# Performance work log

Measured on AMD Instinct MI355X. Metric: run time of the kernel, lower is better.

The kernel has to match this reference:

```python
import jax, jax.numpy as jnp
import numpy as np

N_I, N_O = 100000, 50000   # indivi / org node counts
F = 32                     # node feature dim (both types)
EA = 8                     # edge feature dim
E = 100000                 # edges per relation


def setup_inputs() -> dict:
    key = jax.random.key(0)
    ks = jax.random.split(key, 20)
    s = 0.05
    return {
        "x_indivi": jax.random.normal(ks[0], (N_I, F), jnp.float32),
        "x_org": jax.random.normal(ks[1], (N_O, F), jnp.float32),
        "edge_src_oi": jax.random.randint(ks[2], (E,), 0, N_O),
        "edge_dst_oi": jax.random.randint(ks[3], (E,), 0, N_I),
        "edge_attr_oi": jax.random.normal(ks[4], (E, EA), jnp.float32),
        "edge_src_io": jax.random.randint(ks[5], (E,), 0, N_I),
        "edge_dst_io": jax.random.randint(ks[6], (E,), 0, N_O),
        "edge_attr_io": jax.random.normal(ks[7], (E, EA), jnp.float32),
        "Wm_oi": jax.random.normal(ks[8], (EA, F * F), jnp.float32) * s,
        "bm_oi": jax.random.normal(ks[9], (F * F,), jnp.float32) * s,
        "Wr_oi": jax.random.normal(ks[10], (F, F), jnp.float32) * s,
        "b_oi": jax.random.normal(ks[11], (F,), jnp.float32) * s,
        "Wm_io": jax.random.normal(ks[12], (EA, F * F), jnp.float32) * s,
        "bm_io": jax.random.normal(ks[13], (F * F,), jnp.float32) * s,
        "Wr_io": jax.random.normal(ks[14], (F, F), jnp.float32) * s,
        "b_io": jax.random.normal(ks[15], (F,), jnp.float32) * s,
        "Wm2": jax.random.normal(ks[16], (EA, F * 1), jnp.float32) * s,
        "bm2": jax.random.normal(ks[17], (F * 1,), jnp.float32) * s,
        "Wr2": jax.random.normal(ks[18], (F, 1), jnp.float32) * s,
        "b2": jax.random.normal(ks[19], (1,), jnp.float32) * s,
    }


def nnconv(x_src, x_dst, src, dst, eattr, Wm, bm, Wr, b, f_out):
    # per-edge weight matrix from edge attributes: [E, F_src, f_out]
    w = (eattr @ Wm + bm).reshape(-1, x_src.shape[1], f_out)
    msg = jnp.einsum('ei,eio->eo', x_src[src], w)          # gather + per-edge matmul
    agg = jax.ops.segment_sum(msg, dst, num_segments=x_dst.shape[0])  # scatter-add
    return agg + x_dst @ Wr + b                             # root weight + bias


def reference(x_indivi, x_org, edge_src_oi, edge_dst_oi, edge_attr_oi,
              edge_src_io, edge_dst_io, edge_attr_io,
              Wm_oi, bm_oi, Wr_oi, b_oi,
              Wm_io, bm_io, Wr_io, b_io,
              Wm2, bm2, Wr2, b2):
    # Inner layer: hetero NNConv, aggr='sum' across relations per dst type
    h_indivi = jax.nn.sigmoid(
        nnconv(x_org, x_indivi, edge_src_oi, edge_dst_oi, edge_attr_oi,
               Wm_oi, bm_oi, Wr_oi, b_oi, F))
    h_org = jax.nn.sigmoid(
        nnconv(x_indivi, x_org, edge_src_io, edge_dst_io, edge_attr_io,
               Wm_io, bm_io, Wr_io, b_io, F))
    # Output layer: only relations with dst == 'indivi', out_channels = 1
    out = nnconv(h_org, h_indivi, edge_src_oi, edge_dst_oi, edge_attr_oi,
                 Wm2, bm2, Wr2, b2, 1)
    return jax.nn.sigmoid(out)
```

## Files before the change

kernel.cpp:

```cpp
#include <hip/hip_runtime.h>
#include <math.h>

#define NI 100000
#define NO 50000
#define NE 100000
#define NB (NI + NO)
#define TOTE (2 * NE)

#define OFF_WRT_OI    0
#define OFF_WRT_IO    1024
#define OFF_WFRAG     2048
#define OFF_Y2Z2      11264
#define OFF_SCANNED   611264
#define OFF_BLOCKSUM  761280
#define OFF_BLOCKPREF 761920
#define OFF_SORTED    762560
#define OFF_DSTS      962560
#define OFF_ACC       1162560
#define OFF_CNT       5962560
#define OFF_CNT2      6112576

static constexpr int B_EDGE = (NE + 255) / 256;
static constexpr int B_IND  = (NI + 255) / 256;
static constexpr int B_ORG  = (NO + 255) / 256;
static constexpr int SCAN_BLOCKS = (NB + 255) / 256;

static constexpr int FB_HIST_END  = 782;
static constexpr int FB_ZERO_END  = 1038;
static constexpr int FB_WRT_END   = 1046;
static constexpr int FB_WFRAG_END = 1055;

typedef __attribute__((ext_vector_type(8))) short short8;
typedef __attribute__((ext_vector_type(4))) float f32x4;

__device__ __forceinline__ float sigmoidf_fast(float x) {
    return 1.0f / (1.0f + __expf(-x));
}
__device__ __forceinline__ unsigned f2bf(float f) {
    unsigned u = __float_as_uint(f);
    return (u + 0x7FFFu + ((u >> 16) & 1u)) >> 16;
}
__device__ __forceinline__ unsigned pack_trunc(float lo, float hi) {
    return __builtin_amdgcn_perm(__float_as_uint(hi), __float_as_uint(lo), 0x07060302u);
}

__global__ __launch_bounds__(256) void k_front(
    const int* __restrict__ dst_oi, const int* __restrict__ dst_io,
    const float* __restrict__ Wm_oi, const float* __restrict__ bm_oi, const float* __restrict__ Wr_oi,
    const float* __restrict__ Wm_io, const float* __restrict__ bm_io, const float* __restrict__ Wr_io,
    float* __restrict__ ws, int* __restrict__ cnt)
{
    int b = blockIdx.x;
    if (b < FB_HIST_END) {
        bool is_io = b >= B_EDGE;
        int e = (is_io ? (b - B_EDGE) : b) * 256 + threadIdx.x;
        if (e >= NE) return;
        int cd = is_io ? (NI + dst_io[e]) : dst_oi[e];
        atomicAdd(&cnt[cd], 1);
    } else if (b < FB_ZERO_END) {
        int idx = (b - FB_HIST_END) * 256 + threadIdx.x;
        float4* a4 = (float4*)(ws + OFF_ACC);
        for (int q = idx; q < 1200000; q += 65536)
            a4[q] = make_float4(0.f, 0.f, 0.f, 0.f);
    } else if (b < FB_WRT_END) {
        int u = (b - FB_ZERO_END) * 256 + threadIdx.x;
        if (u < 1024)      ws[OFF_WRT_OI + u] = Wr_oi[(u & 31) * 32 + (u >> 5)];
        else if (u < 2048) { int v = u - 1024; ws[OFF_WRT_IO + v] = Wr_io[(v & 31) * 32 + (v >> 5)]; }
    } else {
        int u = (b - FB_WRT_END) * 256 + threadIdx.x;
        if (u >= 2304) return;
        int rel = u >= 1152;
        int v = u - rel * 1152;
        int lane = v & 63;
        int fi = v >> 6;
        int a = fi >> 1;
        int nt = fi & 1;
        int quad = lane >> 4;
        int n = nt * 16 + (lane & 15);
        const float* Wm = rel ? Wm_io : Wm_oi;
        const float* bm = rel ? bm_io : bm_oi;
        unsigned pk[4];
        #pragma unroll
        for (int d = 0; d < 4; d++) {
            int k0 = quad * 8 + 2 * d;
            float vlo = (a < 8) ? Wm[a * 1024 + k0 * 32 + n]       : bm[k0 * 32 + n];
            float vhi = (a < 8) ? Wm[a * 1024 + (k0 + 1) * 32 + n] : bm[(k0 + 1) * 32 + n];
            pk[d] = f2bf(vlo) | (f2bf(vhi) << 16);
        }
        uint4* wf = (uint4*)(ws + OFF_WFRAG);
        wf[((rel * 9 + a) * 2 + nt) * 64 + lane] = make_uint4(pk[0], pk[1], pk[2], pk[3]);
    }
}

__global__ __launch_bounds__(256) void k_scan_block(
    const int* __restrict__ cnt, int* __restrict__ scanned, int* __restrict__ blocksum)
{
    int d = blockIdx.x * 256 + threadIdx.x;
    int v = (d < NB) ? cnt[d] : 0;
    int lane = threadIdx.x & 63, wv = threadIdx.x >> 6;
    int s = v;
    #pragma unroll
    for (int off = 1; off < 64; off <<= 1) {
        int t = __shfl_up(s, off);
        if (lane >= off) s += t;
    }
    __shared__ int wsum[4];
    if (lane == 63) wsum[wv] = s;
    __syncthreads();
    int add = 0;
    for (int w = 0; w < wv; w++) add += wsum[w];
    int incl = s + add;
    scanned[d] = incl - v;
    if (threadIdx.x == 255) blocksum[blockIdx.x] = incl;
}

__global__ __launch_bounds__(1024) void k_scan_top(
    const int* __restrict__ blocksum, int* __restrict__ blockpref)
{
    __shared__ int L[1024];
    int t = threadIdx.x;
    int v = (t < SCAN_BLOCKS) ? blocksum[t] : 0;
    L[t] = v;
    __syncthreads();
    for (int off = 1; off < 1024; off <<= 1) {
        int u = (t >= off) ? L[t - off] : 0;
        __syncthreads();
        L[t] += u;
        __syncthreads();
    }
    if (t < SCAN_BLOCKS) blockpref[t] = L[t] - v;
}

__global__ __launch_bounds__(256) void k_scatter(
    const int* __restrict__ dst_oi, const int* __restrict__ dst_io,
    const int* __restrict__ scanned, const int* __restrict__ blockpref,
    int* __restrict__ cnt2, int* __restrict__ sorted_eid, int* __restrict__ dstsorted)
{
    bool is_io = blockIdx.x >= B_EDGE;
    int e = (is_io ? (blockIdx.x - B_EDGE) : blockIdx.x) * 256 + threadIdx.x;
    if (e >= NE) return;
    int cd = is_io ? (NI + dst_io[e]) : dst_oi[e];
    int base = scanned[cd] + blockpref[cd >> 8];
    int pos = base + atomicAdd(&cnt2[cd], 1);
    sorted_eid[pos] = e;
    dstsorted[pos] = cd;
}

__global__ __launch_bounds__(256) void k_edge(
    const int* __restrict__ src_oi, const float* __restrict__ attr_oi,
    const int* __restrict__ src_io, const float* __restrict__ attr_io,
    const float* __restrict__ x_ind, const float* __restrict__ x_org,
    const float* __restrict__ ws,
    const int* __restrict__ sorted_eid, const int* __restrict__ dstsorted,
    float* __restrict__ acc)
{
    __shared__ uint4 xstage[4][256];
    __shared__ float stage[256 * 36];

    bool is_io = blockIdx.x >= B_EDGE;
    int blockStart = is_io ? (NE + (blockIdx.x - B_EDGE) * 256) : (blockIdx.x * 256);
    int relEnd = is_io ? TOTE : NE;
    int tid = threadIdx.x;
    int wave = tid >> 6, lane = tid & 63, quad = lane >> 4;
    int p = blockStart + tid;
    bool act = p < relEnd;

    const int*   srcA  = is_io ? src_io : src_oi;
    const float* attrA = is_io ? attr_io : attr_oi;
    const float* xsrc  = is_io ? x_ind : x_org;

    const uint4* wfr = ((const uint4*)(ws + OFF_WFRAG)) + (is_io ? 1152 : 0);
    uint4 bf[9][2];
    #pragma unroll
    for (int a = 0; a < 9; a++) {
        #pragma unroll
        for (int nt = 0; nt < 2; nt++)
            bf[a][nt] = wfr[((a * 2 + nt) * 64) + lane];
    }

    int cd = -1;
    float ar[9];
    ar[8] = 1.0f;
    if (act) {
        cd = dstsorted[p];
        int e = sorted_eid[p];
        int s = srcA[e];
        {
            const float4* ap = (const float4*)(attrA + e * 8);
            float4 v0 = ap[0], v1 = ap[1];
            ar[0] = v0.x; ar[1] = v0.y; ar[2] = v0.z; ar[3] = v0.w;
            ar[4] = v1.x; ar[5] = v1.y; ar[6] = v1.z; ar[7] = v1.w;
        }
        const float4* xp = (const float4*)(xsrc + s * 32);
        #pragma unroll
        for (int q = 0; q < 4; q++) {
            float4 v0 = xp[2 * q], v1 = xp[2 * q + 1];
            uint4 pk;
            pk.x = pack_trunc(v0.x, v0.y);
            pk.y = pack_trunc(v0.z, v0.w);
            pk.z = pack_trunc(v1.x, v1.y);
            pk.w = pack_trunc(v1.z, v1.w);
            xstage[wave][q * 64 + lane] = pk;
        }
    }

    f32x4 zero4 = {0.f, 0.f, 0.f, 0.f};
    #pragma unroll
    for (int mtile = 0; mtile < 4; mtile++) {
        uint4 araw = xstage[wave][quad * 64 + mtile * 16 + (lane & 15)];
        short8 af = *(short8*)&araw;
        float mm0[4] = {0.f, 0.f, 0.f, 0.f};
        float mm1[4] = {0.f, 0.f, 0.f, 0.f};
        #pragma unroll
        for (int a = 0; a < 9; a++) {
            f32x4 t0 = __builtin_amdgcn_mfma_f32_16x16x32_bf16(af, *(short8*)&bf[a][0], zero4, 0, 0, 0);
            f32x4 t1 = __builtin_amdgcn_mfma_f32_16x16x32_bf16(af, *(short8*)&bf[a][1], zero4, 0, 0, 0);
            #pragma unroll
            for (int r = 0; r < 4; r++) {
                int m = mtile * 16 + quad * 4 + r;
                float av = __shfl(ar[a], m, 64);
                mm0[r] = fmaf(av, t0[r], mm0[r]);
                mm1[r] = fmaf(av, t1[r], mm1[r]);
            }
        }
        #pragma unroll
        for (int r = 0; r < 4; r++) {
            int row = wave * 64 + mtile * 16 + quad * 4 + r;
            stage[row * 36 + (lane & 15)]      = mm0[r];
            stage[row * 36 + 16 + (lane & 15)] = mm1[r];
        }
    }
    __syncthreads();

    bool head = act && (p == blockStart || dstsorted[p - 1] != cd);
    if (head) {
        float msg[32];
        const float4* rrow0 = (const float4*)(stage + tid * 36);
        #pragma unroll
        for (int j = 0; j < 8; j++) {
            float4 v = rrow0[j];
            msg[j * 4 + 0] = v.x; msg[j * 4 + 1] = v.y;
            msg[j * 4 + 2] = v.z; msg[j * 4 + 3] = v.w;
        }
        int blockEnd = min(blockStart + 256, relEnd);
        int q = p + 1;
        while (q < blockEnd && dstsorted[q] == cd) {
            const float4* rrow = (const float4*)(stage + (q - blockStart) * 36);
            #pragma unroll
            for (int j = 0; j < 8; j++) {
                float4 v = rrow[j];
                msg[j * 4 + 0] += v.x; msg[j * 4 + 1] += v.y;
                msg[j * 4 + 2] += v.z; msg[j * 4 + 3] += v.w;
            }
            q++;
        }
        bool openR = (q == blockEnd) && (q < TOTE) && (dstsorted[q] == cd);
        bool openL = (p == blockStart) && (p > 0) && (dstsorted[p - 1] == cd);
        float* dp = acc + (size_t)cd * 32;
        if (openL || openR) {
            #pragma unroll
            for (int o = 0; o < 32; o++) atomicAdd(dp + o, msg[o]);
        } else {
            float4* dp4 = (float4*)dp;
            #pragma unroll
            for (int j = 0; j < 8; j++)
                dp4[j] = make_float4(msg[j * 4 + 0], msg[j * 4 + 1], msg[j * 4 + 2], msg[j * 4 + 3]);
        }
    }
}

__global__ __launch_bounds__(256) void k_finish(
    const float* __restrict__ x_ind, const float* __restrict__ x_org,
    const float* __restrict__ ws, const float* __restrict__ acc,
    const float* __restrict__ b_oi, const float* __restrict__ b_io,
    const float* __restrict__ Wm2, const float* __restrict__ bm2,
    const float* __restrict__ Wr2, const float* __restrict__ b2,
    float* __restrict__ y2z2, float* __restrict__ out)
{
    bool is_org = blockIdx.x >= B_IND;
    int n = (is_org ? (blockIdx.x - B_IND) : blockIdx.x) * 256 + threadIdx.x;
    int N = is_org ? NO : NI;
    if (n >= N) return;
    int cd = is_org ? (NI + n) : n;

    const float* x    = is_org ? x_org : x_ind;
    const float* WrT  = ws + (is_org ? OFF_WRT_IO : OFF_WRT_OI);
    const float* bias = is_org ? b_io : b_oi;

    float xr[32];
    const float4* xp = (const float4*)(x + n * 32);
    #pragma unroll
    for (int q = 0; q < 8; q++) {
        float4 v = xp[q];
        xr[q * 4 + 0] = v.x; xr[q * 4 + 1] = v.y; xr[q * 4 + 2] = v.z; xr[q * 4 + 3] = v.w;
    }
    float h[32];
    const float4* aprow = (const float4*)(acc + (size_t)cd * 32);
    #pragma unroll
    for (int q = 0; q < 8; q++) {
        float4 v = aprow[q];
        h[q * 4 + 0] = v.x; h[q * 4 + 1] = v.y; h[q * 4 + 2] = v.z; h[q * 4 + 3] = v.w;
    }
    #pragma unroll 4
    for (int o = 0; o < 32; o++) {
        float s = bias[o] + h[o];
        #pragma unroll
        for (int i = 0; i < 32; i++) s = fmaf(xr[i], WrT[o * 32 + i], s);
        h[o] = sigmoidf_fast(s);
    }
    if (!is_org) {
        float s = b2[0];
        #pragma unroll
        for (int i = 0; i < 32; i++) s = fmaf(h[i], Wr2[i], s);
        out[n] = s;
    } else {
        float z2 = 0.0f;
        #pragma unroll
        for (int i = 0; i < 32; i++) z2 = fmaf(h[i], bm2[i], z2);
        float* yz = y2z2 + n * 12;
        yz[0] = z2;
        #pragma unroll
        for (int a = 0; a < 8; a++) {
            float s = 0.0f;
            #pragma unroll
            for (int i = 0; i < 32; i++) s = fmaf(h[i], Wm2[a * 32 + i], s);
            yz[1 + a] = s;
        }
    }
}

__global__ __launch_bounds__(256) void k_out(
    const int* __restrict__ src_oi, const float* __restrict__ attr_oi,
    const int* __restrict__ scanned, const int* __restrict__ blockpref,
    const int* __restrict__ sorted_eid, const float* __restrict__ y2z2,
    float* __restrict__ out)
{
    int d = blockIdx.x * 256 + threadIdx.x;
    if (d >= NI) return;
    int base = scanned[d] + blockpref[d >> 8];
    int next = scanned[d + 1] + blockpref[(d + 1) >> 8];
    float t = out[d];
    for (int p = base; p < next; p++) {
        int e = sorted_eid[p];
        int s = src_oi[e];
        const float* yz = y2z2 + s * 12;
        const float4* ap = (const float4*)(attr_oi + e * 8);
        float4 a0 = ap[0], a1 = ap[1];
        float m = yz[0];
        m = fmaf(a0.x, yz[1], m); m = fmaf(a0.y, yz[2], m);
        m = fmaf(a0.z, yz[3], m); m = fmaf(a0.w, yz[4], m);
        m = fmaf(a1.x, yz[5], m); m = fmaf(a1.y, yz[6], m);
        m = fmaf(a1.z, yz[7], m); m = fmaf(a1.w, yz[8], m);
        t += m;
    }
    out[d] = sigmoidf_fast(t);
}

extern "C" void kernel_launch(void* const* d_in, const int* in_sizes, int n_in,
                              void* d_out, int out_size, void* d_ws, size_t ws_size,
                              hipStream_t stream)
{
    const float* x_ind   = (const float*)d_in[0];
    const float* x_org   = (const float*)d_in[1];
    const int*   src_oi  = (const int*)d_in[2];
    const int*   dst_oi  = (const int*)d_in[3];
    const float* attr_oi = (const float*)d_in[4];
    const int*   src_io  = (const int*)d_in[5];
    const int*   dst_io  = (const int*)d_in[6];
    const float* attr_io = (const float*)d_in[7];
    const float* Wm_oi   = (const float*)d_in[8];
    const float* bm_oi   = (const float*)d_in[9];
    const float* Wr_oi   = (const float*)d_in[10];
    const float* b_oi    = (const float*)d_in[11];
    const float* Wm_io   = (const float*)d_in[12];
    const float* bm_io   = (const float*)d_in[13];
    const float* Wr_io   = (const float*)d_in[14];
    const float* b_io    = (const float*)d_in[15];
    const float* Wm2     = (const float*)d_in[16];
    const float* bm2     = (const float*)d_in[17];
    const float* Wr2     = (const float*)d_in[18];
    const float* b2      = (const float*)d_in[19];

    float* ws        = (float*)d_ws;
    float* y2z2      = ws + OFF_Y2Z2;
    int*   scanned   = (int*)(ws + OFF_SCANNED);
    int*   blocksum  = (int*)(ws + OFF_BLOCKSUM);
    int*   blockpref = (int*)(ws + OFF_BLOCKPREF);
    int*   sorted    = (int*)(ws + OFF_SORTED);
    int*   dsts      = (int*)(ws + OFF_DSTS);
    float* acc       = ws + OFF_ACC;
    int*   cnt       = (int*)(ws + OFF_CNT);
    int*   cnt2      = (int*)(ws + OFF_CNT2);
    float* out       = (float*)d_out;

    hipMemsetAsync(ws + OFF_CNT, 0, (size_t)(2 * 150016) * 4, stream);

    k_front<<<FB_WFRAG_END, 256, 0, stream>>>(
        dst_oi, dst_io, Wm_oi, bm_oi, Wr_oi, Wm_io, bm_io, Wr_io, ws, cnt);

    k_scan_block<<<SCAN_BLOCKS, 256, 0, stream>>>(cnt, scanned, blocksum);

    k_scan_top<<<1, 1024, 0, stream>>>(blocksum, blockpref);

    k_scatter<<<2 * B_EDGE, 256, 0, stream>>>(
        dst_oi, dst_io, scanned, blockpref, cnt2, sorted, dsts);

    k_edge<<<2 * B_EDGE, 256, 0, stream>>>(
        src_oi, attr_oi, src_io, attr_io, x_ind, x_org, ws, sorted, dsts, acc);

    k_finish<<<B_IND + B_ORG, 256, 0, stream>>>(
        x_ind, x_org, ws, acc, b_oi, b_io, Wm2, bm2, Wr2, b2, y2z2, out);

    k_out<<<B_IND, 256, 0, stream>>>(
        src_oi, attr_oi, scanned, blockpref, sorted, y2z2, out);
}
```

Measured before the change: 184.2 us.

## Fuse scan passes, reuse histogram ranks, and fold indivi finish into output kernel

The histogram kernel now records each edge's atomic rank, so the scatter kernel no longer needs a second atomic counter pass or a second zeroed counter array. The two-level scan becomes a single kernel in which the last block, found through an atomic ticket, scans the block sums. The indivi half of the finish kernel moves into the output kernel, which drops the intermediate out write and read. This cuts launches, atomics and memset size, at the cost of a rank buffer and a heavier per-thread output kernel.

```diff
diff --git a/kernel.cpp b/kernel.cpp
--- a/kernel.cpp
+++ b/kernel.cpp
@@ -16,9 +16,10 @@
 #define OFF_BLOCKPREF 761920
 #define OFF_SORTED    762560
 #define OFF_DSTS      962560
-#define OFF_ACC       1162560
-#define OFF_CNT       5962560
-#define OFF_CNT2      6112576
+#define OFF_RANK      1162560
+#define OFF_ACC       1362560
+#define OFF_CNT       6162560
+#define OFF_TICKET    6312576
 
 static constexpr int B_EDGE = (NE + 255) / 256;
 static constexpr int B_IND  = (NI + 255) / 256;
@@ -48,7 +49,7 @@
     const int* __restrict__ dst_oi, const int* __restrict__ dst_io,
     const float* __restrict__ Wm_oi, const float* __restrict__ bm_oi, const float* __restrict__ Wr_oi,
     const float* __restrict__ Wm_io, const float* __restrict__ bm_io, const float* __restrict__ Wr_io,
-    float* __restrict__ ws, int* __restrict__ cnt)
+    float* __restrict__ ws, int* __restrict__ cnt, int* __restrict__ rank)
 {
     int b = blockIdx.x;
     if (b < FB_HIST_END) {
@@ -56,7 +57,7 @@
         int e = (is_io ? (b - B_EDGE) : b) * 256 + threadIdx.x;
         if (e >= NE) return;
         int cd = is_io ? (NI + dst_io[e]) : dst_oi[e];
-        atomicAdd(&cnt[cd], 1);
+        rank[is_io ? NE + e : e] = atomicAdd(&cnt[cd], 1);
     } else if (b < FB_ZERO_END) {
         int idx = (b - FB_HIST_END) * 256 + threadIdx.x;
         float4* a4 = (float4*)(ws + OFF_ACC);
@@ -92,8 +93,9 @@
     }
 }
 
-__global__ __launch_bounds__(256) void k_scan_block(
-    const int* __restrict__ cnt, int* __restrict__ scanned, int* __restrict__ blocksum)
+__global__ __launch_bounds__(256) void k_scan(
+    const int* __restrict__ cnt, int* __restrict__ scanned,
+    int* __restrict__ blocksum, int* __restrict__ blockpref, int* __restrict__ ticket)
 {
     int d = blockIdx.x * 256 + threadIdx.x;
     int v = (d < NB) ? cnt[d] : 0;
@@ -109,39 +111,55 @@
     __syncthreads();
     int add = 0;
     for (int w = 0; w < wv; w++) add += wsum[w];
-    int incl = s + add;
-    scanned[d] = incl - v;
-    if (threadIdx.x == 255) blocksum[blockIdx.x] = incl;
-}
-
-__global__ __launch_bounds__(1024) void k_scan_top(
-    const int* __restrict__ blocksum, int* __restrict__ blockpref)
-{
-    __shared__ int L[1024];
+    scanned[d] = s + add - v;
+
+    __shared__ int isLast;
+    if (threadIdx.x == 0) {
+        int total = wsum[0] + wsum[1] + wsum[2] + wsum[3];
+        blocksum[blockIdx.x] = total;
+        __threadfence();
+        isLast = (atomicAdd(ticket, 1) == (int)gridDim.x - 1);
+    }
+    __syncthreads();
+    if (!isLast) return;
+    __threadfence();
+
+    __shared__ int L[768];
     int t = threadIdx.x;
-    int v = (t < SCAN_BLOCKS) ? blocksum[t] : 0;
-    L[t] = v;
+    #pragma unroll
+    for (int j = 0; j < 3; j++) {
+        int i = t * 3 + j;
+        L[t * 3 + j] = (i < SCAN_BLOCKS) ? blocksum[i] : 0;
+    }
     __syncthreads();
-    for (int off = 1; off < 1024; off <<= 1) {
-        int u = (t >= off) ? L[t - off] : 0;
-        __syncthreads();
-        L[t] += u;
-        __syncthreads();
-    }
-    if (t < SCAN_BLOCKS) blockpref[t] = L[t] - v;
+    int s0 = L[t * 3], s1 = s0 + L[t * 3 + 1], s2 = s1 + L[t * 3 + 2];
+    int sc = s2;
+    #pragma unroll
+    for (int off = 1; off < 64; off <<= 1) {
+        int u = __shfl_up(sc, off);
+        if (lane >= off) sc += u;
+    }
+    __shared__ int wsum2[4];
+    if (lane == 63) wsum2[wv] = sc;
+    __syncthreads();
+    int add2 = 0;
+    for (int w = 0; w < wv; w++) add2 += wsum2[w];
+    int excl = sc + add2 - s2;
+    if (t * 3     < SCAN_BLOCKS) blockpref[t * 3]     = excl;
+    if (t * 3 + 1 < SCAN_BLOCKS) blockpref[t * 3 + 1] = excl + s0;
+    if (t * 3 + 2 < SCAN_BLOCKS) blockpref[t * 3 + 2] = excl + s1;
 }
 
 __global__ __launch_bounds__(256) void k_scatter(
     const int* __restrict__ dst_oi, const int* __restrict__ dst_io,
     const int* __restrict__ scanned, const int* __restrict__ blockpref,
-    int* __restrict__ cnt2, int* __restrict__ sorted_eid, int* __restrict__ dstsorted)
+    const int* __restrict__ rank, int* __restrict__ sorted_eid, int* __restrict__ dstsorted)
 {
     bool is_io = blockIdx.x >= B_EDGE;
     int e = (is_io ? (blockIdx.x - B_EDGE) : blockIdx.x) * 256 + threadIdx.x;
     if (e >= NE) return;
     int cd = is_io ? (NI + dst_io[e]) : dst_oi[e];
-    int base = scanned[cd] + blockpref[cd >> 8];
-    int pos = base + atomicAdd(&cnt2[cd], 1);
+    int pos = scanned[cd] + blockpref[cd >> 8] + rank[is_io ? NE + e : e];
     sorted_eid[pos] = e;
     dstsorted[pos] = cd;
 }
@@ -269,26 +287,19 @@
     }
 }
 
-__global__ __launch_bounds__(256) void k_finish(
-    const float* __restrict__ x_ind, const float* __restrict__ x_org,
-    const float* __restrict__ ws, const float* __restrict__ acc,
-    const float* __restrict__ b_oi, const float* __restrict__ b_io,
+__global__ __launch_bounds__(256) void k_finish_org(
+    const float* __restrict__ x_org, const float* __restrict__ ws, const float* __restrict__ acc,
+    const float* __restrict__ b_io,
     const float* __restrict__ Wm2, const float* __restrict__ bm2,
-    const float* __restrict__ Wr2, const float* __restrict__ b2,
-    float* __restrict__ y2z2, float* __restrict__ out)
-{
-    bool is_org = blockIdx.x >= B_IND;
-    int n = (is_org ? (blockIdx.x - B_IND) : blockIdx.x) * 256 + threadIdx.x;
-    int N = is_org ? NO : NI;
-    if (n >= N) return;
-    int cd = is_org ? (NI + n) : n;
-
-    const float* x    = is_org ? x_org : x_ind;
-    const float* WrT  = ws + (is_org ? OFF_WRT_IO : OFF_WRT_OI);
-    const float* bias = is_org ? b_io : b_oi;
+    float* __restrict__ y2z2)
+{
+    int n = blockIdx.x * 256 + threadIdx.x;
+    if (n >= NO) return;
+    int cd = NI + n;
+    const float* WrT = ws + OFF_WRT_IO;
 
     float xr[32];
-    const float4* xp = (const float4*)(x + n * 32);
+    const float4* xp = (const float4*)(x_org + n * 32);
     #pragma unroll
     for (int q = 0; q < 8; q++) {
         float4 v = xp[q];
@@ -303,33 +314,29 @@
     }
     #pragma unroll 4
     for (int o = 0; o < 32; o++) {
-        float s = bias[o] + h[o];
+        float s = b_io[o] + h[o];
         #pragma unroll
         for (int i = 0; i < 32; i++) s = fmaf(xr[i], WrT[o * 32 + i], s);
         h[o] = sigmoidf_fast(s);
     }
-    if (!is_org) {
-        float s = b2[0];
-        #pragma unroll
-        for (int i = 0; i < 32; i++) s = fmaf(h[i], Wr2[i], s);
-        out[n] = s;
-    } else {
-        float z2 = 0.0f;
-        #pragma unroll
-        for (int i = 0; i < 32; i++) z2 = fmaf(h[i], bm2[i], z2);
-        float* yz = y2z2 + n * 12;
-        yz[0] = z2;
-        #pragma unroll
-        for (int a = 0; a < 8; a++) {
-            float s = 0.0f;
-            #pragma unroll
-            for (int i = 0; i < 32; i++) s = fmaf(h[i], Wm2[a * 32 + i], s);
-            yz[1 + a] = s;
-        }
+    float z2 = 0.0f;
+    #pragma unroll
+    for (int i = 0; i < 32; i++) z2 = fmaf(h[i], bm2[i], z2);
+    float* yz = y2z2 + n * 12;
+    yz[0] = z2;
+    #pragma unroll
+    for (int a = 0; a < 8; a++) {
+        float s = 0.0f;
+        #pragma unroll
+        for (int i = 0; i < 32; i++) s = fmaf(h[i], Wm2[a * 32 + i], s);
+        yz[1 + a] = s;
     }
 }
 
 __global__ __launch_bounds__(256) void k_out(
+    const float* __restrict__ x_ind, const float* __restrict__ ws, const float* __restrict__ acc,
+    const float* __restrict__ b_oi,
+    const float* __restrict__ Wr2, const float* __restrict__ b2,
     const int* __restrict__ src_oi, const float* __restrict__ attr_oi,
     const int* __restrict__ scanned, const int* __restrict__ blockpref,
     const int* __restrict__ sorted_eid, const float* __restrict__ y2z2,
@@ -337,9 +344,33 @@
 {
     int d = blockIdx.x * 256 + threadIdx.x;
     if (d >= NI) return;
+    const float* WrT = ws + OFF_WRT_OI;
+
+    float xr[32];
+    const float4* xp = (const float4*)(x_ind + d * 32);
+    #pragma unroll
+    for (int q = 0; q < 8; q++) {
+        float4 v = xp[q];
+        xr[q * 4 + 0] = v.x; xr[q * 4 + 1] = v.y; xr[q * 4 + 2] = v.z; xr[q * 4 + 3] = v.w;
+    }
+    float h[32];
+    const float4* aprow = (const float4*)(acc + (size_t)d * 32);
+    #pragma unroll
+    for (int q = 0; q < 8; q++) {
+        float4 v = aprow[q];
+        h[q * 4 + 0] = v.x; h[q * 4 + 1] = v.y; h[q * 4 + 2] = v.z; h[q * 4 + 3] = v.w;
+    }
+    float t = b2[0];
+    #pragma unroll 4
+    for (int o = 0; o < 32; o++) {
+        float s = b_oi[o] + h[o];
+        #pragma unroll
+        for (int i = 0; i < 32; i++) s = fmaf(xr[i], WrT[o * 32 + i], s);
+        t = fmaf(sigmoidf_fast(s), Wr2[o], t);
+    }
+
     int base = scanned[d] + blockpref[d >> 8];
     int next = scanned[d + 1] + blockpref[(d + 1) >> 8];
-    float t = out[d];
     for (int p = base; p < next; p++) {
         int e = sorted_eid[p];
         int s = src_oi[e];
@@ -388,29 +419,29 @@
     int*   blockpref = (int*)(ws + OFF_BLOCKPREF);
     int*   sorted    = (int*)(ws + OFF_SORTED);
     int*   dsts      = (int*)(ws + OFF_DSTS);
+    int*   rank      = (int*)(ws + OFF_RANK);
     float* acc       = ws + OFF_ACC;
     int*   cnt       = (int*)(ws + OFF_CNT);
-    int*   cnt2      = (int*)(ws + OFF_CNT2);
+    int*   ticket    = (int*)(ws + OFF_TICKET);
     float* out       = (float*)d_out;
 
-    hipMemsetAsync(ws + OFF_CNT, 0, (size_t)(2 * 150016) * 4, stream);
+    hipMemsetAsync(ws + OFF_CNT, 0, (size_t)(150016 + 16) * 4, stream);
 
     k_front<<<FB_WFRAG_END, 256, 0, stream>>>(
-        dst_oi, dst_io, Wm_oi, bm_oi, Wr_oi, Wm_io, bm_io, Wr_io, ws, cnt);
-
-    k_scan_block<<<SCAN_BLOCKS, 256, 0, stream>>>(cnt, scanned, blocksum);
-
-    k_scan_top<<<1, 1024, 0, stream>>>(blocksum, blockpref);
+        dst_oi, dst_io, Wm_oi, bm_oi, Wr_oi, Wm_io, bm_io, Wr_io, ws, cnt, rank);
+
+    k_scan<<<SCAN_BLOCKS, 256, 0, stream>>>(cnt, scanned, blocksum, blockpref, ticket);
 
     k_scatter<<<2 * B_EDGE, 256, 0, stream>>>(
-        dst_oi, dst_io, scanned, blockpref, cnt2, sorted, dsts);
+        dst_oi, dst_io, scanned, blockpref, rank, sorted, dsts);
 
     k_edge<<<2 * B_EDGE, 256, 0, stream>>>(
         src_oi, attr_oi, src_io, attr_io, x_ind, x_org, ws, sorted, dsts, acc);
 
-    k_finish<<<B_IND + B_ORG, 256, 0, stream>>>(
-        x_ind, x_org, ws, acc, b_oi, b_io, Wm2, bm2, Wr2, b2, y2z2, out);
+    k_finish_org<<<B_ORG, 256, 0, stream>>>(
+        x_org, ws, acc, b_io, Wm2, bm2, y2z2);
 
     k_out<<<B_IND, 256, 0, stream>>>(
-        src_oi, attr_oi, scanned, blockpref, sorted, y2z2, out);
-}
+        x_ind, ws, acc, b_oi, Wr2, b2, src_oi, attr_oi,
+        scanned, blockpref, sorted, y2z2, out);
+}
```

Result: slower. 202.3 us (+9.8%).

## Replace counting-sort CSR with atomic linked lists and per-edge message buffer

Applied to the files above, without the earlier changes.

Drops the histogram, two-level scan and scatter kernels that built a destination-sorted edge order. Instead, the message kernel pushes each edge onto a per-destination linked list with atomicExch and writes its 32-float message to a global buffer. Per-node kernels then walk the lists to sum messages, and the root and bias math is fused into the org and output kernels. This cuts several launches and the sort passes, at the cost of writing and re-reading a 25.6MB message buffer, serial pointer-chasing gathers per node, and nondeterministic summation order.

```diff
diff --git a/kernel.cpp b/kernel.cpp
--- a/kernel.cpp
+++ b/kernel.cpp
@@ -7,28 +7,16 @@
 #define NB (NI + NO)
 #define TOTE (2 * NE)
 
-#define OFF_WRT_OI    0
-#define OFF_WRT_IO    1024
-#define OFF_WFRAG     2048
-#define OFF_Y2Z2      11264
-#define OFF_SCANNED   611264
-#define OFF_BLOCKSUM  761280
-#define OFF_BLOCKPREF 761920
-#define OFF_SORTED    762560
-#define OFF_DSTS      962560
-#define OFF_ACC       1162560
-#define OFF_CNT       5962560
-#define OFF_CNT2      6112576
+#define OFF_WFRAG   0
+#define OFF_Y2Z2    9216
+#define OFF_HEAD    609216
+#define OFF_NXT     759232
+#define OFF_MSG     959232
 
 static constexpr int B_EDGE = (NE + 255) / 256;
 static constexpr int B_IND  = (NI + 255) / 256;
 static constexpr int B_ORG  = (NO + 255) / 256;
-static constexpr int SCAN_BLOCKS = (NB + 255) / 256;
-
-static constexpr int FB_HIST_END  = 782;
-static constexpr int FB_ZERO_END  = 1038;
-static constexpr int FB_WRT_END   = 1046;
-static constexpr int FB_WFRAG_END = 1055;
+static constexpr int B_INIT = (NB + 2304 + 255) / 256;
 
 typedef __attribute__((ext_vector_type(8))) short short8;
 typedef __attribute__((ext_vector_type(4))) float f32x4;
@@ -44,30 +32,17 @@
     return __builtin_amdgcn_perm(__float_as_uint(hi), __float_as_uint(lo), 0x07060302u);
 }
 
-__global__ __launch_bounds__(256) void k_front(
-    const int* __restrict__ dst_oi, const int* __restrict__ dst_io,
-    const float* __restrict__ Wm_oi, const float* __restrict__ bm_oi, const float* __restrict__ Wr_oi,
-    const float* __restrict__ Wm_io, const float* __restrict__ bm_io, const float* __restrict__ Wr_io,
-    float* __restrict__ ws, int* __restrict__ cnt)
-{
-    int b = blockIdx.x;
-    if (b < FB_HIST_END) {
-        bool is_io = b >= B_EDGE;
-        int e = (is_io ? (b - B_EDGE) : b) * 256 + threadIdx.x;
-        if (e >= NE) return;
-        int cd = is_io ? (NI + dst_io[e]) : dst_oi[e];
-        atomicAdd(&cnt[cd], 1);
-    } else if (b < FB_ZERO_END) {
-        int idx = (b - FB_HIST_END) * 256 + threadIdx.x;
-        float4* a4 = (float4*)(ws + OFF_ACC);
-        for (int q = idx; q < 1200000; q += 65536)
-            a4[q] = make_float4(0.f, 0.f, 0.f, 0.f);
-    } else if (b < FB_WRT_END) {
-        int u = (b - FB_ZERO_END) * 256 + threadIdx.x;
-        if (u < 1024)      ws[OFF_WRT_OI + u] = Wr_oi[(u & 31) * 32 + (u >> 5)];
-        else if (u < 2048) { int v = u - 1024; ws[OFF_WRT_IO + v] = Wr_io[(v & 31) * 32 + (v >> 5)]; }
+__global__ __launch_bounds__(256) void k_init(
+    const float* __restrict__ Wm_oi, const float* __restrict__ bm_oi,
+    const float* __restrict__ Wm_io, const float* __restrict__ bm_io,
+    float* __restrict__ ws)
+{
+    int idx = blockIdx.x * 256 + threadIdx.x;
+    int* head = (int*)(ws + OFF_HEAD);
+    if (idx < NB) {
+        head[idx] = -1;
     } else {
-        int u = (b - FB_WRT_END) * 256 + threadIdx.x;
+        int u = idx - NB;
         if (u >= 2304) return;
         int rel = u >= 1152;
         int v = u - rel * 1152;
@@ -92,80 +67,30 @@
     }
 }
 
-__global__ __launch_bounds__(256) void k_scan_block(
-    const int* __restrict__ cnt, int* __restrict__ scanned, int* __restrict__ blocksum)
-{
-    int d = blockIdx.x * 256 + threadIdx.x;
-    int v = (d < NB) ? cnt[d] : 0;
-    int lane = threadIdx.x & 63, wv = threadIdx.x >> 6;
-    int s = v;
-    #pragma unroll
-    for (int off = 1; off < 64; off <<= 1) {
-        int t = __shfl_up(s, off);
-        if (lane >= off) s += t;
-    }
-    __shared__ int wsum[4];
-    if (lane == 63) wsum[wv] = s;
-    __syncthreads();
-    int add = 0;
-    for (int w = 0; w < wv; w++) add += wsum[w];
-    int incl = s + add;
-    scanned[d] = incl - v;
-    if (threadIdx.x == 255) blocksum[blockIdx.x] = incl;
-}
-
-__global__ __launch_bounds__(1024) void k_scan_top(
-    const int* __restrict__ blocksum, int* __restrict__ blockpref)
-{
-    __shared__ int L[1024];
-    int t = threadIdx.x;
-    int v = (t < SCAN_BLOCKS) ? blocksum[t] : 0;
-    L[t] = v;
-    __syncthreads();
-    for (int off = 1; off < 1024; off <<= 1) {
-        int u = (t >= off) ? L[t - off] : 0;
-        __syncthreads();
-        L[t] += u;
-        __syncthreads();
-    }
-    if (t < SCAN_BLOCKS) blockpref[t] = L[t] - v;
-}
-
-__global__ __launch_bounds__(256) void k_scatter(
-    const int* __restrict__ dst_oi, const int* __restrict__ dst_io,
-    const int* __restrict__ scanned, const int* __restrict__ blockpref,
-    int* __restrict__ cnt2, int* __restrict__ sorted_eid, int* __restrict__ dstsorted)
-{
-    bool is_io = blockIdx.x >= B_EDGE;
-    int e = (is_io ? (blockIdx.x - B_EDGE) : blockIdx.x) * 256 + threadIdx.x;
-    if (e >= NE) return;
-    int cd = is_io ? (NI + dst_io[e]) : dst_oi[e];
-    int base = scanned[cd] + blockpref[cd >> 8];
-    int pos = base + atomicAdd(&cnt2[cd], 1);
-    sorted_eid[pos] = e;
-    dstsorted[pos] = cd;
-}
-
-__global__ __launch_bounds__(256) void k_edge(
-    const int* __restrict__ src_oi, const float* __restrict__ attr_oi,
-    const int* __restrict__ src_io, const float* __restrict__ attr_io,
+__global__ __launch_bounds__(256) void k_msg(
+    const int* __restrict__ src_oi, const int* __restrict__ dst_oi, const float* __restrict__ attr_oi,
+    const int* __restrict__ src_io, const int* __restrict__ dst_io, const float* __restrict__ attr_io,
     const float* __restrict__ x_ind, const float* __restrict__ x_org,
-    const float* __restrict__ ws,
-    const int* __restrict__ sorted_eid, const int* __restrict__ dstsorted,
-    float* __restrict__ acc)
+    float* __restrict__ ws)
 {
     __shared__ uint4 xstage[4][256];
     __shared__ float stage[256 * 36];
 
+    int* head  = (int*)(ws + OFF_HEAD);
+    int* nxt   = (int*)(ws + OFF_NXT);
+    float* msg = ws + OFF_MSG;
+
     bool is_io = blockIdx.x >= B_EDGE;
-    int blockStart = is_io ? (NE + (blockIdx.x - B_EDGE) * 256) : (blockIdx.x * 256);
+    int blockStart = is_io ? (NE + ((int)blockIdx.x - B_EDGE) * 256) : ((int)blockIdx.x * 256);
     int relEnd = is_io ? TOTE : NE;
     int tid = threadIdx.x;
     int wave = tid >> 6, lane = tid & 63, quad = lane >> 4;
     int p = blockStart + tid;
     bool act = p < relEnd;
+    int e = p - (is_io ? NE : 0);
 
     const int*   srcA  = is_io ? src_io : src_oi;
+    const int*   dstA  = is_io ? dst_io : dst_oi;
     const float* attrA = is_io ? attr_io : attr_oi;
     const float* xsrc  = is_io ? x_ind : x_org;
 
@@ -178,12 +103,9 @@
             bf[a][nt] = wfr[((a * 2 + nt) * 64) + lane];
     }
 
-    int cd = -1;
     float ar[9];
     ar[8] = 1.0f;
     if (act) {
-        cd = dstsorted[p];
-        int e = sorted_eid[p];
         int s = srcA[e];
         {
             const float4* ap = (const float4*)(attrA + e * 8);
@@ -202,6 +124,9 @@
             pk.w = pack_trunc(v1.z, v1.w);
             xstage[wave][q * 64 + lane] = pk;
         }
+        int cd = is_io ? (NI + dstA[e]) : dstA[e];
+        int old = atomicExch(&head[cd], p);
+        nxt[p] = old;
     }
 
     f32x4 zero4 = {0.f, 0.f, 0.f, 0.f};
@@ -232,116 +157,93 @@
     }
     __syncthreads();
 
-    bool head = act && (p == blockStart || dstsorted[p - 1] != cd);
-    if (head) {
-        float msg[32];
-        const float4* rrow0 = (const float4*)(stage + tid * 36);
+    if (act) {
+        const float4* srow = (const float4*)(stage + tid * 36);
+        float4* mrow = (float4*)(msg + (size_t)p * 32);
+        #pragma unroll
+        for (int j = 0; j < 8; j++) mrow[j] = srow[j];
+    }
+}
+
+__global__ __launch_bounds__(256) void k_org(
+    const float* __restrict__ x_org, const float* __restrict__ ws,
+    const float* __restrict__ Wr_io, const float* __restrict__ b_io,
+    const float* __restrict__ Wm2, const float* __restrict__ bm2,
+    float* __restrict__ y2z2)
+{
+    int n = blockIdx.x * 256 + threadIdx.x;
+    if (n >= NO) return;
+    const int* head  = (const int*)(ws + OFF_HEAD);
+    const int* nxt   = (const int*)(ws + OFF_NXT);
+    const float* msg = ws + OFF_MSG;
+
+    float ms[32];
+    #pragma unroll
+    for (int o = 0; o < 32; o++) ms[o] = 0.0f;
+    for (int e = head[NI + n]; e != -1; e = nxt[e]) {
+        const float4* mr = (const float4*)(msg + (size_t)e * 32);
         #pragma unroll
         for (int j = 0; j < 8; j++) {
-            float4 v = rrow0[j];
-            msg[j * 4 + 0] = v.x; msg[j * 4 + 1] = v.y;
-            msg[j * 4 + 2] = v.z; msg[j * 4 + 3] = v.w;
-        }
-        int blockEnd = min(blockStart + 256, relEnd);
-        int q = p + 1;
-        while (q < blockEnd && dstsorted[q] == cd) {
-            const float4* rrow = (const float4*)(stage + (q - blockStart) * 36);
-            #pragma unroll
-            for (int j = 0; j < 8; j++) {
-                float4 v = rrow[j];
-                msg[j * 4 + 0] += v.x; msg[j * 4 + 1] += v.y;
-                msg[j * 4 + 2] += v.z; msg[j * 4 + 3] += v.w;
-            }
-            q++;
-        }
-        bool openR = (q == blockEnd) && (q < TOTE) && (dstsorted[q] == cd);
-        bool openL = (p == blockStart) && (p > 0) && (dstsorted[p - 1] == cd);
-        float* dp = acc + (size_t)cd * 32;
-        if (openL || openR) {
-            #pragma unroll
-            for (int o = 0; o < 32; o++) atomicAdd(dp + o, msg[o]);
-        } else {
-            float4* dp4 = (float4*)dp;
-            #pragma unroll
-            for (int j = 0; j < 8; j++)
-                dp4[j] = make_float4(msg[j * 4 + 0], msg[j * 4 + 1], msg[j * 4 + 2], msg[j * 4 + 3]);
-        }
-    }
-}
-
-__global__ __launch_bounds__(256) void k_finish(
-    const float* __restrict__ x_ind, const float* __restrict__ x_org,
-    const float* __restrict__ ws, const float* __restrict__ acc,
-    const float* __restrict__ b_oi, const float* __restrict__ b_io,
-    const float* __restrict__ Wm2, const float* __restrict__ bm2,
-    const float* __restrict__ Wr2, const float* __restrict__ b2,
-    float* __restrict__ y2z2, float* __restrict__ out)
-{
-    bool is_org = blockIdx.x >= B_IND;
-    int n = (is_org ? (blockIdx.x - B_IND) : blockIdx.x) * 256 + threadIdx.x;
-    int N = is_org ? NO : NI;
-    if (n >= N) return;
-    int cd = is_org ? (NI + n) : n;
-
-    const float* x    = is_org ? x_org : x_ind;
-    const float* WrT  = ws + (is_org ? OFF_WRT_IO : OFF_WRT_OI);
-    const float* bias = is_org ? b_io : b_oi;
-
+            float4 v = mr[j];
+            ms[j * 4 + 0] += v.x; ms[j * 4 + 1] += v.y;
+            ms[j * 4 + 2] += v.z; ms[j * 4 + 3] += v.w;
+        }
+    }
     float xr[32];
-    const float4* xp = (const float4*)(x + n * 32);
+    const float4* xp = (const float4*)(x_org + n * 32);
     #pragma unroll
     for (int q = 0; q < 8; q++) {
         float4 v = xp[q];
         xr[q * 4 + 0] = v.x; xr[q * 4 + 1] = v.y; xr[q * 4 + 2] = v.z; xr[q * 4 + 3] = v.w;
     }
     float h[32];
-    const float4* aprow = (const float4*)(acc + (size_t)cd * 32);
-    #pragma unroll
-    for (int q = 0; q < 8; q++) {
-        float4 v = aprow[q];
-        h[q * 4 + 0] = v.x; h[q * 4 + 1] = v.y; h[q * 4 + 2] = v.z; h[q * 4 + 3] = v.w;
-    }
     #pragma unroll 4
     for (int o = 0; o < 32; o++) {
-        float s = bias[o] + h[o];
-        #pragma unroll
-        for (int i = 0; i < 32; i++) s = fmaf(xr[i], WrT[o * 32 + i], s);
+        float s = b_io[o] + ms[o];
+        #pragma unroll
+        for (int i = 0; i < 32; i++) s = fmaf(xr[i], Wr_io[i * 32 + o], s);
         h[o] = sigmoidf_fast(s);
     }
-    if (!is_org) {
-        float s = b2[0];
-        #pragma unroll
-        for (int i = 0; i < 32; i++) s = fmaf(h[i], Wr2[i], s);
-        out[n] = s;
-    } else {
-        float z2 = 0.0f;
-        #pragma unroll
-        for (int i = 0; i < 32; i++) z2 = fmaf(h[i], bm2[i], z2);
-        float* yz = y2z2 + n * 12;
-        yz[0] = z2;
-        #pragma unroll
-        for (int a = 0; a < 8; a++) {
-            float s = 0.0f;
-            #pragma unroll
-            for (int i = 0; i < 32; i++) s = fmaf(h[i], Wm2[a * 32 + i], s);
-            yz[1 + a] = s;
-        }
+    float z2 = 0.0f;
+    #pragma unroll
+    for (int i = 0; i < 32; i++) z2 = fmaf(h[i], bm2[i], z2);
+    float* yz = y2z2 + n * 12;
+    yz[0] = z2;
+    #pragma unroll
+    for (int a = 0; a < 8; a++) {
+        float s = 0.0f;
+        #pragma unroll
+        for (int i = 0; i < 32; i++) s = fmaf(h[i], Wm2[a * 32 + i], s);
+        yz[1 + a] = s;
     }
 }
 
 __global__ __launch_bounds__(256) void k_out(
+    const float* __restrict__ x_ind, const float* __restrict__ ws,
+    const float* __restrict__ Wr_oi, const float* __restrict__ b_oi,
     const int* __restrict__ src_oi, const float* __restrict__ attr_oi,
-    const int* __restrict__ scanned, const int* __restrict__ blockpref,
-    const int* __restrict__ sorted_eid, const float* __restrict__ y2z2,
+    const float* __restrict__ Wr2, const float* __restrict__ b2,
+    const float* __restrict__ y2z2,
     float* __restrict__ out)
 {
     int d = blockIdx.x * 256 + threadIdx.x;
     if (d >= NI) return;
-    int base = scanned[d] + blockpref[d >> 8];
-    int next = scanned[d + 1] + blockpref[(d + 1) >> 8];
-    float t = out[d];
-    for (int p = base; p < next; p++) {
-        int e = sorted_eid[p];
+    const int* head  = (const int*)(ws + OFF_HEAD);
+    const int* nxt   = (const int*)(ws + OFF_NXT);
+    const float* msg = ws + OFF_MSG;
+
+    float ms[32];
+    #pragma unroll
+    for (int o = 0; o < 32; o++) ms[o] = 0.0f;
+    float m2acc = 0.0f;
+    for (int e = head[d]; e != -1; e = nxt[e]) {
+        const float4* mr = (const float4*)(msg + (size_t)e * 32);
+        #pragma unroll
+        for (int j = 0; j < 8; j++) {
+            float4 v = mr[j];
+            ms[j * 4 + 0] += v.x; ms[j * 4 + 1] += v.y;
+            ms[j * 4 + 2] += v.z; ms[j * 4 + 3] += v.w;
+        }
         int s = src_oi[e];
         const float* yz = y2z2 + s * 12;
         const float4* ap = (const float4*)(attr_oi + e * 8);
@@ -351,7 +253,22 @@
         m = fmaf(a0.z, yz[3], m); m = fmaf(a0.w, yz[4], m);
         m = fmaf(a1.x, yz[5], m); m = fmaf(a1.y, yz[6], m);
         m = fmaf(a1.z, yz[7], m); m = fmaf(a1.w, yz[8], m);
-        t += m;
+        m2acc += m;
+    }
+    float xr[32];
+    const float4* xp = (const float4*)(x_ind + d * 32);
+    #pragma unroll
+    for (int q = 0; q < 8; q++) {
+        float4 v = xp[q];
+        xr[q * 4 + 0] = v.x; xr[q * 4 + 1] = v.y; xr[q * 4 + 2] = v.z; xr[q * 4 + 3] = v.w;
+    }
+    float t = b2[0] + m2acc;
+    #pragma unroll 4
+    for (int o = 0; o < 32; o++) {
+        float s = b_oi[o] + ms[o];
+        #pragma unroll
+        for (int i = 0; i < 32; i++) s = fmaf(xr[i], Wr_oi[i * 32 + o], s);
+        t = fmaf(sigmoidf_fast(s), Wr2[o], t);
     }
     out[d] = sigmoidf_fast(t);
 }
@@ -381,36 +298,18 @@
     const float* Wr2     = (const float*)d_in[18];
     const float* b2      = (const float*)d_in[19];
 
-    float* ws        = (float*)d_ws;
-    float* y2z2      = ws + OFF_Y2Z2;
-    int*   scanned   = (int*)(ws + OFF_SCANNED);
-    int*   blocksum  = (int*)(ws + OFF_BLOCKSUM);
-    int*   blockpref = (int*)(ws + OFF_BLOCKPREF);
-    int*   sorted    = (int*)(ws + OFF_SORTED);
-    int*   dsts      = (int*)(ws + OFF_DSTS);
-    float* acc       = ws + OFF_ACC;
-    int*   cnt       = (int*)(ws + OFF_CNT);
-    int*   cnt2      = (int*)(ws + OFF_CNT2);
-    float* out       = (float*)d_out;
-
-    hipMemsetAsync(ws + OFF_CNT, 0, (size_t)(2 * 150016) * 4, stream);
-
-    k_front<<<FB_WFRAG_END, 256, 0, stream>>>(
-        dst_oi, dst_io, Wm_oi, bm_oi, Wr_oi, Wm_io, bm_io, Wr_io, ws, cnt);
-
-    k_scan_block<<<SCAN_BLOCKS, 256, 0, stream>>>(cnt, scanned, blocksum);
-
-    k_scan_top<<<1, 1024, 0, stream>>>(blocksum, blockpref);
-
-    k_scatter<<<2 * B_EDGE, 256, 0, stream>>>(
-        dst_oi, dst_io, scanned, blockpref, cnt2, sorted, dsts);
-
-    k_edge<<<2 * B_EDGE, 256, 0, stream>>>(
-        src_oi, attr_oi, src_io, attr_io, x_ind, x_org, ws, sorted, dsts, acc);
-
-    k_finish<<<B_IND + B_ORG, 256, 0, stream>>>(
-        x_ind, x_org, ws, acc, b_oi, b_io, Wm2, bm2, Wr2, b2, y2z2, out);
+    float* ws   = (float*)d_ws;
+    float* y2z2 = ws + OFF_Y2Z2;
+    float* out  = (float*)d_out;
+
+    k_init<<<B_INIT, 256, 0, stream>>>(Wm_oi, bm_oi, Wm_io, bm_io, ws);
+
+    k_msg<<<2 * B_EDGE, 256, 0, stream>>>(
+        src_oi, dst_oi, attr_oi, src_io, dst_io, attr_io, x_ind, x_org, ws);
+
+    k_org<<<B_ORG, 256, 0, stream>>>(
+        x_org, ws, Wr_io, b_io, Wm2, bm2, y2z2);
 
     k_out<<<B_IND, 256, 0, stream>>>(
-        src_oi, attr_oi, scanned, blockpref, sorted, y2z2, out);
-}
+        x_ind, ws, Wr_oi, b_oi, src_oi, attr_oi, Wr2, b2, y2z2, out);
+}
```

Measured after the change: 166.6 us. 1.11x faster.
